# Performance work log

Measured on AMD Instinct MI355X. Metric: run time of the kernel, lower is better.

The kernel has to match this reference:

```python
import jax, jax.numpy as jnp
import numpy as np

V, E, D, B = 8192, 48, 64, 256  # nodes, hyperedges, feat dim, graphs (32 nodes/graph)


def setup_inputs() -> dict:
    key = jax.random.key(0)
    k1, k2, k3, k4 = jax.random.split(key, 4)
    x = jax.random.normal(k1, (V, D), dtype=jnp.float32)
    H = (jax.random.uniform(k2, (V, E)) < 0.3).astype(jnp.float32)
    W = jax.random.normal(k3, (D, D), dtype=jnp.float32) / np.sqrt(D)
    b = jax.random.normal(k4, (D,), dtype=jnp.float32) * 0.01
    # equal-sized graphs: node i belongs to graph i // (V//B)
    batch = jnp.repeat(jnp.arange(B, dtype=jnp.int32), V // B)
    return {"x": x, "H": H, "W": W, "b": b, "batch": batch, "num_graphs": B}


def reference(x, H, W, b, batch, num_graphs):
    Vn, Dd = x.shape
    Ee = H.shape[1]
    # edge_emb_tensor = x.unsqueeze(1) * H.unsqueeze(2)  -> (V, E, d)
    edge_emb = x[:, None, :] * H[:, :, None]
    # scatter mean over nodes by graph id -> (B, E, d)
    counts = jax.ops.segment_sum(jnp.ones((Vn,), x.dtype), batch, num_segments=num_graphs)
    sums = jax.ops.segment_sum(edge_emb.reshape(Vn, Ee * Dd), batch, num_segments=num_graphs)
    edge_dim = (sums / counts[:, None]).reshape(num_graphs, Ee, Dd)
    # MLP f: Linear(d,d) + ReLU (torch Linear: x @ W.T + b)
    edge_dim = jax.nn.relu(jnp.einsum('bed,fd->bef', edge_dim, W) + b)
    # repeat_interleave by per-graph node counts == gather by batch index -> (V, E, d)
    node_emb = (edge_dim[batch] * H[:, :, None]).mean(axis=1)  # (V, d)
    h_e = edge_dim.reshape(num_graphs * Ee, Dd)
    # global mean pool over nodes per graph -> (B, d)
    c = jax.ops.segment_sum(node_emb, batch, num_segments=num_graphs) / counts[:, None]
    return c, h_e
```

## Files before the change

kernel.cpp:

```cpp
#include <hip/hip_runtime.h>

constexpr int V   = 8192;
constexpr int E   = 48;
constexpr int D   = 64;
constexpr int B   = 256;
constexpr int NPG = 32;
constexpr int THREADS = 512, WAVES = 8;
constexpr int EPW = E / WAVES;
constexpr int RPW = NPG / WAVES;

__global__ __launch_bounds__(THREADS) void hgnn_kernel(
    const float* __restrict__ x,
    const float* __restrict__ Hm,
    const float* __restrict__ W,
    const float* __restrict__ b,
    float* __restrict__ out_c,
    float* __restrict__ out_he)
{
    __shared__ float x_lds[NPG][D];
    __shared__ float H_lin[NPG * E];
    __shared__ float Ht[E][NPG];
    __shared__ float P_lds[NPG][D];
    __shared__ float cpart[WAVES][D];

    const int g    = blockIdx.x;
    const int t    = threadIdx.x;
    const int lane = t & 63;
    const int wave = t >> 6;

    float4 wreg[16];
    const float4* Wrow = reinterpret_cast<const float4*>(W + (size_t)lane * D);
    #pragma unroll
    for (int k = 0; k < 16; ++k) wreg[k] = Wrow[k];

    reinterpret_cast<float4*>(&x_lds[0][0])[t] =
        reinterpret_cast<const float4*>(x + (size_t)g * NPG * D)[t];
    if (t < 384)
        reinterpret_cast<float4*>(H_lin)[t] =
            reinterpret_cast<const float4*>(Hm + (size_t)g * NPG * E)[t];
    const float bb = b[lane];
    __syncthreads();

    #pragma unroll
    for (int k = 0; k < 3; ++k) {
        int j = t + k * THREADS;
        int e = j >> 5, v = j & 31;
        Ht[e][v] = H_lin[v * E + e];
    }

    {
        float acc[RPW] = {0.f, 0.f, 0.f, 0.f};
        #pragma unroll
        for (int k = 0; k < 16; ++k) {
            const float4 w4 = wreg[k];
            #pragma unroll
            for (int r = 0; r < RPW; ++r) {
                const float4 x4 =
                    reinterpret_cast<const float4*>(&x_lds[wave * RPW + r][0])[k];
                acc[r] += x4.x * w4.x + x4.y * w4.y + x4.z * w4.z + x4.w * w4.w;
            }
        }
        #pragma unroll
        for (int r = 0; r < RPW; ++r)
            P_lds[wave * RPW + r][lane] = acc[r];
    }
    __syncthreads();

    float y[EPW], hs[EPW];
    #pragma unroll
    for (int i = 0; i < EPW; ++i) { y[i] = 0.f; hs[i] = 0.f; }
    const int e0 = wave * EPW;
    #pragma unroll
    for (int k = 0; k < NPG / 4; ++k) {
        float4 p4;
        p4.x = P_lds[4 * k + 0][lane];
        p4.y = P_lds[4 * k + 1][lane];
        p4.z = P_lds[4 * k + 2][lane];
        p4.w = P_lds[4 * k + 3][lane];
        #pragma unroll
        for (int i = 0; i < EPW; ++i) {
            const float4 h4 = reinterpret_cast<const float4*>(&Ht[e0 + i][0])[k];
            y[i]  += h4.x * p4.x + h4.y * p4.y + h4.z * p4.z + h4.w * p4.w;
            hs[i] += (h4.x + h4.y) + (h4.z + h4.w);
        }
    }
    float csum = 0.f;
    #pragma unroll
    for (int i = 0; i < EPW; ++i) {
        float yv = fmaxf(y[i] * (1.f / NPG) + bb, 0.f);
        out_he[((size_t)g * E + e0 + i) * D + lane] = yv;
        csum += yv * hs[i];
    }
    cpart[wave][lane] = csum;
    __syncthreads();

    if (t < D) {
        float c = 0.f;
        #pragma unroll
        for (int w = 0; w < WAVES; ++w) c += cpart[w][t];
        out_c[(size_t)g * D + t] = c * (1.f / (NPG * E));
    }
}

extern "C" void kernel_launch(void* const* d_in, const int* in_sizes, int n_in,
                              void* d_out, int out_size, void* d_ws, size_t ws_size,
                              hipStream_t stream) {
    (void)in_sizes; (void)n_in; (void)d_ws; (void)ws_size; (void)out_size;
    const float* x  = (const float*)d_in[0];
    const float* Hm = (const float*)d_in[1];
    const float* W  = (const float*)d_in[2];
    const float* b  = (const float*)d_in[3];
    float* out    = (float*)d_out;
    float* out_c  = out;
    float* out_he = out + B * D;
    hgnn_kernel<<<B, THREADS, 0, stream>>>(x, Hm, W, b, out_c, out_he);
}
```

Before: 14.68 us.

## Read x directly from global and transpose H on load, dropping a barrier

The x tile is no longer staged in LDS. Each wave reads its rows straight from global memory as wave-uniform broadcast loads, using readfirstlane to make the wave index scalar. H is transposed into LDS as it is loaded, which removes the intermediate linear buffer and one __syncthreads. The per-edge H column sums are computed once by 48 threads from global memory instead of inside the inner loop. This shortens the load/sync chain in front of the matmul, but the 48 serial column-sum reads and the repeated global x loads could add latency.

```diff
diff --git a/kernel.cpp b/kernel.cpp
--- a/kernel.cpp
+++ b/kernel.cpp
@@ -17,59 +17,57 @@
     float* __restrict__ out_c,
     float* __restrict__ out_he)
 {
-    __shared__ float x_lds[NPG][D];
-    __shared__ float H_lin[NPG * E];
     __shared__ float Ht[E][NPG];
     __shared__ float P_lds[NPG][D];
+    __shared__ float hsl[E];
     __shared__ float cpart[WAVES][D];
 
     const int g    = blockIdx.x;
     const int t    = threadIdx.x;
     const int lane = t & 63;
-    const int wave = t >> 6;
+    const int wu   = __builtin_amdgcn_readfirstlane(t >> 6);
 
     float4 wreg[16];
     const float4* Wrow = reinterpret_cast<const float4*>(W + (size_t)lane * D);
     #pragma unroll
     for (int k = 0; k < 16; ++k) wreg[k] = Wrow[k];
 
-    reinterpret_cast<float4*>(&x_lds[0][0])[t] =
-        reinterpret_cast<const float4*>(x + (size_t)g * NPG * D)[t];
-    if (t < 384)
-        reinterpret_cast<float4*>(H_lin)[t] =
-            reinterpret_cast<const float4*>(Hm + (size_t)g * NPG * E)[t];
+    if (t < 384) {
+        int v = t / 12, e4 = (t % 12) * 4;
+        float4 h4 = *reinterpret_cast<const float4*>(Hm + ((size_t)g * NPG + v) * E + e4);
+        Ht[e4 + 0][v] = h4.x;
+        Ht[e4 + 1][v] = h4.y;
+        Ht[e4 + 2][v] = h4.z;
+        Ht[e4 + 3][v] = h4.w;
+    }
+    if (t < E) {
+        float s = 0.f;
+        #pragma unroll
+        for (int v = 0; v < NPG; ++v) s += Hm[((size_t)g * NPG + v) * E + t];
+        hsl[t] = s;
+    }
     const float bb = b[lane];
-    __syncthreads();
-
-    #pragma unroll
-    for (int k = 0; k < 3; ++k) {
-        int j = t + k * THREADS;
-        int e = j >> 5, v = j & 31;
-        Ht[e][v] = H_lin[v * E + e];
-    }
 
     {
+        const float* xg = x + ((size_t)g * NPG + wu * RPW) * D;
         float acc[RPW] = {0.f, 0.f, 0.f, 0.f};
         #pragma unroll
         for (int k = 0; k < 16; ++k) {
             const float4 w4 = wreg[k];
             #pragma unroll
             for (int r = 0; r < RPW; ++r) {
-                const float4 x4 =
-                    reinterpret_cast<const float4*>(&x_lds[wave * RPW + r][0])[k];
+                const float4 x4 = reinterpret_cast<const float4*>(xg + r * D)[k];
                 acc[r] += x4.x * w4.x + x4.y * w4.y + x4.z * w4.z + x4.w * w4.w;
             }
         }
         #pragma unroll
         for (int r = 0; r < RPW; ++r)
-            P_lds[wave * RPW + r][lane] = acc[r];
+            P_lds[wu * RPW + r][lane] = acc[r];
     }
     __syncthreads();
 
-    float y[EPW], hs[EPW];
-    #pragma unroll
-    for (int i = 0; i < EPW; ++i) { y[i] = 0.f; hs[i] = 0.f; }
-    const int e0 = wave * EPW;
+    const int e0 = wu * EPW;
+    float y[EPW] = {};
     #pragma unroll
     for (int k = 0; k < NPG / 4; ++k) {
         float4 p4;
@@ -80,8 +78,7 @@
         #pragma unroll
         for (int i = 0; i < EPW; ++i) {
             const float4 h4 = reinterpret_cast<const float4*>(&Ht[e0 + i][0])[k];
-            y[i]  += h4.x * p4.x + h4.y * p4.y + h4.z * p4.z + h4.w * p4.w;
-            hs[i] += (h4.x + h4.y) + (h4.z + h4.w);
+            y[i] += h4.x * p4.x + h4.y * p4.y + h4.z * p4.z + h4.w * p4.w;
         }
     }
     float csum = 0.f;
@@ -89,9 +86,9 @@
     for (int i = 0; i < EPW; ++i) {
         float yv = fmaxf(y[i] * (1.f / NPG) + bb, 0.f);
         out_he[((size_t)g * E + e0 + i) * D + lane] = yv;
-        csum += yv * hs[i];
+        csum += yv * hsl[e0 + i];
     }
-    cpart[wave][lane] = csum;
+    cpart[wu][lane] = csum;
     __syncthreads();
 
     if (t < D) {
```

Result: slower. 15.54 us (+5.9%).
